# Kernel optimization log

Hardware: AMD Instinct MI355X
Metric: run time of the kernel (lower is better)

The kernel has to match this reference:

```python
import jax, jax.numpy as jnp
import numpy as np

B, N, D, O, L = 16, 2000, 128, 64, 3  # batch, n_nodes, hidden_dim, output_dim, n_layers


def _init(key, shape, fan_in):
    return jax.random.normal(key, shape, jnp.float32) / np.sqrt(fan_in).astype(np.float32)


def setup_inputs() -> dict:
    key = jax.random.key(0)
    ks = jax.random.split(key, 8)
    return {
        "coords": jax.random.normal(ks[0], (B, N, 2), jnp.float32),
        "enc_w0": _init(ks[1], (2, D), 2),
        "enc_b0": jnp.zeros((D,), jnp.float32),
        "enc_w1": _init(ks[2], (D, D), D),
        "enc_b1": jnp.zeros((D,), jnp.float32),
        "gat_W": _init(ks[3], (L, D, D), D),      # per-layer GAT projection (no bias)
        "gat_a1": _init(ks[4], (L, D), 2 * D),    # first half of attention vector a
        "gat_a2": _init(ks[5], (L, D), 2 * D),    # second half of attention vector a
        "proj_w": _init(ks[6], (D, O), D),
        "proj_b": jnp.zeros((O,), jnp.float32),
    }


def _leaky(x):
    return jnp.where(x >= 0, x, 0.2 * x)  # LeakyReLU(0.2)


def reference(coords, enc_w0, enc_b0, enc_w1, enc_b1, gat_W, gat_a1, gat_a2, proj_w, proj_b):
    # node encoder: Linear -> ReLU -> Linear
    h = jax.nn.relu(coords @ enc_w0 + enc_b0) @ enc_w1 + enc_b1  # [B,N,D]
    n_layers = gat_W.shape[0]
    for l in range(n_layers):
        Wh = h @ gat_W[l]                      # [B,N,D]
        # additive GAT attention: e_ij = leakyrelu(a1.Wh_i + a2.Wh_j)
        # (equivalent to a([Wh_i || Wh_j]) without materializing N*N*2D tensor)
        e1 = Wh @ gat_a1[l]                    # [B,N]
        e2 = Wh @ gat_a2[l]                    # [B,N]
        e = _leaky(e1[:, :, None] + e2[:, None, :])  # [B,N,N]
        # adj is all-ones in forward() so the masked_fill is a no-op
        att = jax.nn.softmax(e, axis=-1)       # [B,N,N]; dropout is identity (eval)
        h = jax.nn.relu(att @ Wh)              # [B,N,D]
    return h @ proj_w + proj_b                 # [B,N,O]
```

## Files before the change

kernel.cpp:

```cpp
#include <hip/hip_runtime.h>
#include <hip/hip_bf16.h>

using bf16 = __hip_bfloat16;

#define BATCH 16
#define NNODE 2000
#define DIM   128
#define ODIM  64
#define NLAYER 3
#define BN    (BATCH*NNODE)
#define NP1   (NNODE+1)
#define CHK   125
#define CKS   16

#define OFF_COORDS 0
#define OFF_EW0    64000
#define OFF_EB0    64256
#define OFF_EW1    64384
#define OFF_EB1    80768
#define OFF_GW     80896
#define OFF_GA1    130048
#define OFF_GA2    130432
#define OFF_PW     130816
#define OFF_PB     139008
#define CVT_TOT    139072

struct InPtrs { const void* p[10]; };

__global__ void convert_all_k(InPtrs in, float* __restrict__ dst, float* __restrict__ flag)
{
    __shared__ int scnt[256];
    const unsigned short* raw = (const unsigned short*)in.p[0];
    int t = threadIdx.x, c = 0;
    for (int k = t; k < 2048; k += 256){
        unsigned short u = raw[2*k];
        int e = (u >> 7) & 0xFF;
        if (e >= 100 && e <= 140) ++c;
    }
    scnt[t] = c;
    __syncthreads();
    for (int s = 128; s; s >>= 1){ if (t < s) scnt[t] += scnt[t+s]; __syncthreads(); }
    const bool isbf16 = (scnt[0] >= 1800);
    if (blockIdx.x == 0 && t == 0) flag[0] = isbf16 ? 1.0f : 0.0f;

    const int off[11] = {OFF_COORDS,OFF_EW0,OFF_EB0,OFF_EW1,OFF_EB1,
                         OFF_GW,OFF_GA1,OFF_GA2,OFF_PW,OFF_PB,CVT_TOT};
    int i = blockIdx.x*256 + t;
    if (i >= CVT_TOT) return;
    int seg = 0;
    #pragma unroll
    for (int s = 1; s < 10; ++s) if (i >= off[s]) seg = s;
    int li = i - off[seg];
    if (isbf16) dst[i] = __bfloat162float(((const bf16*)in.p[seg])[li]);
    else        dst[i] = ((const float*)in.p[seg])[li];
}

__global__ __launch_bounds__(256) void encgemm_k(const float* __restrict__ cvt,
                                                 float* __restrict__ out)
{
    __shared__ __align__(16) float sW[128*64];
    __shared__ __align__(16) float sA[32*128];
    const int rt = blockIdx.x, cb = blockIdx.y, tid = threadIdx.x;
    const float* W      = cvt + OFF_EW1;
    const float* bias   = cvt + OFF_EB1;
    const float* coords = cvt + OFF_COORDS;
    const float* w0     = cvt + OFF_EW0;
    const float* b0v    = cvt + OFF_EB0;

    for (int e = tid; e < 128*64; e += 256){
        int k = e >> 6, cc = e & 63;
        sW[e] = W[k*DIM + cb*64 + cc];
    }
    for (int e = tid; e < 32*128; e += 256){
        int r = e >> 7, k = e & 127;
        int node = rt*32 + r;
        float c0 = coords[node*2+0], c1 = coords[node*2+1];
        float v = fmaf(c0, w0[k], fmaf(c1, w0[DIM+k], b0v[k]));
        sA[e] = v > 0.f ? v : 0.f;
    }
    __syncthreads();

    const int cq = tid & 15, rr = tid >> 4;
    float4 acc0 = make_float4(0.f,0.f,0.f,0.f);
    float4 acc1 = make_float4(0.f,0.f,0.f,0.f);
    for (int kq = 0; kq < 32; ++kq){
        float4 w0q = *(float4*)&sW[(kq*4+0)*64 + cq*4];
        float4 w1q = *(float4*)&sW[(kq*4+1)*64 + cq*4];
        float4 w2q = *(float4*)&sW[(kq*4+2)*64 + cq*4];
        float4 w3q = *(float4*)&sW[(kq*4+3)*64 + cq*4];
        float4 a0 = *(float4*)&sA[rr*128 + kq*4];
        float4 a1 = *(float4*)&sA[(rr+16)*128 + kq*4];
        acc0.x = fmaf(a0.x,w0q.x, fmaf(a0.y,w1q.x, fmaf(a0.z,w2q.x, fmaf(a0.w,w3q.x, acc0.x))));
        acc0.y = fmaf(a0.x,w0q.y, fmaf(a0.y,w1q.y, fmaf(a0.z,w2q.y, fmaf(a0.w,w3q.y, acc0.y))));
        acc0.z = fmaf(a0.x,w0q.z, fmaf(a0.y,w1q.z, fmaf(a0.z,w2q.z, fmaf(a0.w,w3q.z, acc0.z))));
        acc0.w = fmaf(a0.x,w0q.w, fmaf(a0.y,w1q.w, fmaf(a0.z,w2q.w, fmaf(a0.w,w3q.w, acc0.w))));
        acc1.x = fmaf(a1.x,w0q.x, fmaf(a1.y,w1q.x, fmaf(a1.z,w2q.x, fmaf(a1.w,w3q.x, acc1.x))));
        acc1.y = fmaf(a1.x,w0q.y, fmaf(a1.y,w1q.y, fmaf(a1.z,w2q.y, fmaf(a1.w,w3q.y, acc1.y))));
        acc1.z = fmaf(a1.x,w0q.z, fmaf(a1.y,w1q.z, fmaf(a1.z,w2q.z, fmaf(a1.w,w3q.z, acc1.z))));
        acc1.w = fmaf(a1.x,w0q.w, fmaf(a1.y,w1q.w, fmaf(a1.z,w2q.w, fmaf(a1.w,w3q.w, acc1.w))));
    }
    const int col0 = cb*64 + cq*4;
    float b0=bias[col0], b1=bias[col0+1], b2=bias[col0+2], b3=bias[col0+3];
    int r0 = rt*32 + rr;
    *(float4*)&out[(size_t)r0*DIM + col0]      = make_float4(acc0.x+b0, acc0.y+b1, acc0.z+b2, acc0.w+b3);
    *(float4*)&out[(size_t)(r0+16)*DIM + col0] = make_float4(acc1.x+b0, acc1.y+b1, acc1.z+b2, acc1.w+b3);
}

__global__ __launch_bounds__(256) void gatgemm_k(const float* __restrict__ A,
    const float* __restrict__ W, const float* __restrict__ a1, const float* __restrict__ a2,
    float* __restrict__ out, float* __restrict__ e1p, float* __restrict__ e2p)
{
    __shared__ __align__(16) float sW[128*64];
    __shared__ __align__(16) float sA[32*128];
    const int rt = blockIdx.x, cb = blockIdx.y, tid = threadIdx.x;

    for (int e = tid; e < 128*64; e += 256){
        int k = e >> 6, cc = e & 63;
        sW[e] = W[k*DIM + cb*64 + cc];
    }
    const float4* Ab = (const float4*)(A + (size_t)rt*32*128);
    float4* sA4 = (float4*)sA;
    for (int q = tid; q < 32*32; q += 256) sA4[q] = Ab[q];
    __syncthreads();

    const int cq = tid & 15, rr = tid >> 4;
    float4 acc0 = make_float4(0.f,0.f,0.f,0.f);
    float4 acc1 = make_float4(0.f,0.f,0.f,0.f);
    for (int kq = 0; kq < 32; ++kq){
        float4 w0q = *(float4*)&sW[(kq*4+0)*64 + cq*4];
        float4 w1q = *(float4*)&sW[(kq*4+1)*64 + cq*4];
        float4 w2q = *(float4*)&sW[(kq*4+2)*64 + cq*4];
        float4 w3q = *(float4*)&sW[(kq*4+3)*64 + cq*4];
        float4 a0 = *(float4*)&sA[rr*128 + kq*4];
        float4 a1q = *(float4*)&sA[(rr+16)*128 + kq*4];
        acc0.x = fmaf(a0.x,w0q.x, fmaf(a0.y,w1q.x, fmaf(a0.z,w2q.x, fmaf(a0.w,w3q.x, acc0.x))));
        acc0.y = fmaf(a0.x,w0q.y, fmaf(a0.y,w1q.y, fmaf(a0.z,w2q.y, fmaf(a0.w,w3q.y, acc0.y))));
        acc0.z = fmaf(a0.x,w0q.z, fmaf(a0.y,w1q.z, fmaf(a0.z,w2q.z, fmaf(a0.w,w3q.z, acc0.z))));
        acc0.w = fmaf(a0.x,w0q.w, fmaf(a0.y,w1q.w, fmaf(a0.z,w2q.w, fmaf(a0.w,w3q.w, acc0.w))));
        acc1.x = fmaf(a1q.x,w0q.x, fmaf(a1q.y,w1q.x, fmaf(a1q.z,w2q.x, fmaf(a1q.w,w3q.x, acc1.x))));
        acc1.y = fmaf(a1q.x,w0q.y, fmaf(a1q.y,w1q.y, fmaf(a1q.z,w2q.y, fmaf(a1q.w,w3q.y, acc1.y))));
        acc1.z = fmaf(a1q.x,w0q.z, fmaf(a1q.y,w1q.z, fmaf(a1q.z,w2q.z, fmaf(a1q.w,w3q.z, acc1.z))));
        acc1.w = fmaf(a1q.x,w0q.w, fmaf(a1q.y,w1q.w, fmaf(a1q.z,w2q.w, fmaf(a1q.w,w3q.w, acc1.w))));
    }
    const int col0 = cb*64 + cq*4;
    int r0 = rt*32 + rr;
    *(float4*)&out[(size_t)r0*DIM + col0]      = acc0;
    *(float4*)&out[(size_t)(r0+16)*DIM + col0] = acc1;

    float a1v0=a1[col0], a1v1=a1[col0+1], a1v2=a1[col0+2], a1v3=a1[col0+3];
    float a2v0=a2[col0], a2v1=a2[col0+1], a2v2=a2[col0+2], a2v3=a2[col0+3];
    float p1r0 = acc0.x*a1v0 + acc0.y*a1v1 + acc0.z*a1v2 + acc0.w*a1v3;
    float p2r0 = acc0.x*a2v0 + acc0.y*a2v1 + acc0.z*a2v2 + acc0.w*a2v3;
    float p1r1 = acc1.x*a1v0 + acc1.y*a1v1 + acc1.z*a1v2 + acc1.w*a1v3;
    float p2r1 = acc1.x*a2v0 + acc1.y*a2v1 + acc1.z*a2v2 + acc1.w*a2v3;
    #pragma unroll
    for (int msk = 1; msk < 16; msk <<= 1){
        p1r0 += __shfl_xor(p1r0, msk); p2r0 += __shfl_xor(p2r0, msk);
        p1r1 += __shfl_xor(p1r1, msk); p2r1 += __shfl_xor(p2r1, msk);
    }
    if (cq == 0){
        e1p[cb*BN + r0]    = p1r0;  e2p[cb*BN + r0]    = p2r0;
        e1p[cb*BN + r0+16] = p1r1;  e2p[cb*BN + r0+16] = p2r1;
    }
}

__global__ __launch_bounds__(256) void gemmout_k(const float* __restrict__ A,
    const float* __restrict__ W, const float* __restrict__ bias,
    void* __restrict__ outp, const float* __restrict__ flag)
{
    __shared__ __align__(16) float sW[128*64];
    __shared__ __align__(16) float sA[32*128];
    const int rt = blockIdx.x, tid = threadIdx.x;
    for (int e = tid; e < 128*64; e += 256){
        int k = e >> 6, cc = e & 63;
        sW[e] = W[k*ODIM + cc];
    }
    const float4* Ab = (const float4*)(A + (size_t)rt*32*128);
    float4* sA4 = (float4*)sA;
    for (int q = tid; q < 32*32; q += 256) sA4[q] = Ab[q];
    __syncthreads();

    const int cq = tid & 15, rr = tid >> 4;
    float4 acc0 = make_float4(0.f,0.f,0.f,0.f);
    float4 acc1 = make_float4(0.f,0.f,0.f,0.f);
    for (int kq = 0; kq < 32; ++kq){
        float4 w0q = *(float4*)&sW[(kq*4+0)*64 + cq*4];
        float4 w1q = *(float4*)&sW[(kq*4+1)*64 + cq*4];
        float4 w2q = *(float4*)&sW[(kq*4+2)*64 + cq*4];
        float4 w3q = *(float4*)&sW[(kq*4+3)*64 + cq*4];
        float4 a0 = *(float4*)&sA[rr*128 + kq*4];
        float4 a1 = *(float4*)&sA[(rr+16)*128 + kq*4];
        acc0.x = fmaf(a0.x,w0q.x, fmaf(a0.y,w1q.x, fmaf(a0.z,w2q.x, fmaf(a0.w,w3q.x, acc0.x))));
        acc0.y = fmaf(a0.x,w0q.y, fmaf(a0.y,w1q.y, fmaf(a0.z,w2q.y, fmaf(a0.w,w3q.y, acc0.y))));
        acc0.z = fmaf(a0.x,w0q.z, fmaf(a0.y,w1q.z, fmaf(a0.z,w2q.z, fmaf(a0.w,w3q.z, acc0.z))));
        acc0.w = fmaf(a0.x,w0q.w, fmaf(a0.y,w1q.w, fmaf(a0.z,w2q.w, fmaf(a0.w,w3q.w, acc0.w))));
        acc1.x = fmaf(a1.x,w0q.x, fmaf(a1.y,w1q.x, fmaf(a1.z,w2q.x, fmaf(a1.w,w3q.x, acc1.x))));
        acc1.y = fmaf(a1.x,w0q.y, fmaf(a1.y,w1q.y, fmaf(a1.z,w2q.y, fmaf(a1.w,w3q.y, acc1.y))));
        acc1.z = fmaf(a1.x,w0q.z, fmaf(a1.y,w1q.z, fmaf(a1.z,w2q.z, fmaf(a1.w,w3q.z, acc1.z))));
        acc1.w = fmaf(a1.x,w0q.w, fmaf(a1.y,w1q.w, fmaf(a1.z,w2q.w, fmaf(a1.w,w3q.w, acc1.w))));
    }
    const int col0 = cq*4;
    float b0=bias[col0], b1=bias[col0+1], b2=bias[col0+2], b3=bias[col0+3];
    float o0[4] = {acc0.x+b0, acc0.y+b1, acc0.z+b2, acc0.w+b3};
    float o1[4] = {acc1.x+b0, acc1.y+b1, acc1.z+b2, acc1.w+b3};
    int r0 = rt*32 + rr;
    size_t p0 = (size_t)r0*ODIM + col0, p1 = (size_t)(r0+16)*ODIM + col0;
    if (flag[0] != 0.0f){
        bf16* ob = (bf16*)outp;
        #pragma unroll
        for (int i = 0; i < 4; ++i){ ob[p0+i] = __float2bfloat16(o0[i]); ob[p1+i] = __float2bfloat16(o1[i]); }
    } else {
        float* of = (float*)outp;
        *(float4*)&of[p0] = make_float4(o0[0],o0[1],o0[2],o0[3]);
        *(float4*)&of[p1] = make_float4(o1[0],o1[1],o1[2],o1[3]);
    }
}

#define WAVE_FENCE() __asm__ volatile("" ::: "memory")
__global__ void sort_k(const float* __restrict__ e2p, float* __restrict__ e2s, int* __restrict__ sidx,
                       float* __restrict__ wp, float* __restrict__ wn, float* __restrict__ e2m)
{
    __shared__ float v[2048];
    __shared__ int  ix[2048];
    const int b = blockIdx.x, t = threadIdx.x;
    for (int i = t; i < 2048; i += 1024){
        v[i]  = (i < NNODE) ? (e2p[b*NNODE + i] + e2p[BN + b*NNODE + i]) : 3.0e38f;
        ix[i] = i;
    }
    __syncthreads();

    #pragma unroll 1
    for (int size = 2; size <= 128; size <<= 1){
        #pragma unroll 1
        for (int stride = size >> 1; stride > 0; stride >>= 1){
            int i = 2*t - (t & (stride-1));
            int j = i + stride;
            bool asc = ((i & size) == 0);
            float vi = v[i], vj = v[j];
            bool sw = asc ? (vi > vj) : (vi < vj);
            if (sw){ v[i]=vj; v[j]=vi; int tm=ix[i]; ix[i]=ix[j]; ix[j]=tm; }
            WAVE_FENCE();
        }
    }
    __syncthreads();

    #pragma unroll 1
    for (int size = 256; size <= 2048; size <<= 1){
        #pragma unroll 1
        for (int stride = size >> 1; stride >= 128; stride >>= 1){
            int i = 2*t - (t & (stride-1));
            int j = i + stride;
            bool asc = ((i & size) == 0);
            float vi = v[i], vj = v[j];
            bool sw = asc ? (vi > vj) : (vi < vj);
            if (sw){ v[i]=vj; v[j]=vi; int tm=ix[i]; ix[i]=ix[j]; ix[j]=tm; }
            __syncthreads();
        }
        #pragma unroll 1
        for (int stride = 64; stride > 0; stride >>= 1){
            int i = 2*t - (t & (stride-1));
            int j = i + stride;
            bool asc = ((i & size) == 0);
            float vi = v[i], vj = v[j];
            bool sw = asc ? (vi > vj) : (vi < vj);
            if (sw){ v[i]=vj; v[j]=vi; int tm=ix[i]; ix[i]=ix[j]; ix[j]=tm; }
            WAVE_FENCE();
        }
        __syncthreads();
    }

    float mx = v[NNODE-1];
    for (int i = t; i < NNODE; i += 1024){
        float val = v[i];
        e2s [b*NNODE+i] = val;
        sidx[b*NNODE+i] = ix[i];
        wp  [b*NNODE+i] = __expf(val - mx);
        wn  [b*NNODE+i] = __expf(0.2f*(val - mx));
    }
    if (t == 0) e2m[b] = mx;
}

__global__ void passA_k(const float* __restrict__ Wh, const int* __restrict__ sidx,
    const float* __restrict__ wp, const float* __restrict__ wn,
    float* __restrict__ chunkP, float* __restrict__ chunkN,
    float* __restrict__ schunkP, float* __restrict__ schunkN)
{
    const int b = blockIdx.x / CHK, c = blockIdx.x % CHK, d = threadIdx.x;
    const int base = b*NNODE;
    float sp=0.f, sn=0.f, ssp=0.f, ssn=0.f;
    #pragma unroll 4
    for (int r = c*CKS; r < c*CKS + CKS; ++r){
        int j = sidx[base + r];
        float whv = Wh[((size_t)base + j)*DIM + d];
        float wpv = wp[base + r], wnv = wn[base + r];
        sp = fmaf(wpv, whv, sp);  sn = fmaf(wnv, whv, sn);
        ssp += wpv;  ssn += wnv;
    }
    const int idx = b*CHK + c;
    chunkP[idx*DIM + d] = sp;
    chunkN[idx*DIM + d] = sn;
    if (d == 0){ schunkP[idx] = ssp; schunkN[idx] = ssn; }
}

__global__ __launch_bounds__(256) void passB_k(
    const float* __restrict__ chunkP, const float* __restrict__ chunkN,
    const float* __restrict__ schunkP, const float* __restrict__ schunkN,
    float* __restrict__ offP, float* __restrict__ offN,
    float* __restrict__ soffP, float* __restrict__ soffN)
{
    const int b = blockIdx.x, tid = threadIdx.x;
    const bool doP = (blockIdx.y == 0);
    const float* chunk  = doP ? chunkP  : chunkN;
    const float* schunk = doP ? schunkP : schunkN;
    float* off  = doP ? offP  : offN;
    float* soff = doP ? soffP : soffN;

    if (tid < 128){
        const int d = tid;
        float acc = 0.f, v[25];
        #pragma unroll
        for (int t = 0; t < 5; ++t){
            const int c0 = doP ? (4-t)*25 : t*25;
            #pragma unroll
            for (int k = 0; k < 25; ++k) v[k] = chunk[(b*CHK + c0 + k)*DIM + d];
            if (doP){
                #pragma unroll
                for (int k = 24; k >= 0; --k){ off[(b*CHK + c0 + k)*DIM + d] = acc; acc += v[k]; }
            } else {
                #pragma unroll
                for (int k = 0; k < 25; ++k){ off[(b*CHK + c0 + k)*DIM + d] = acc; acc += v[k]; }
            }
        }
    } else if (tid == 128){
        float sacc = 0.f, sv[25];
        #pragma unroll
        for (int t = 0; t < 5; ++t){
            const int c0 = doP ? (4-t)*25 : t*25;
            #pragma unroll
            for (int k = 0; k < 25; ++k) sv[k] = schunk[b*CHK + c0 + k];
            if (doP){
                #pragma unroll
                for (int k = 24; k >= 0; --k){ soff[b*CHK + c0 + k] = sacc; sacc += sv[k]; }
            } else {
                #pragma unroll
                for (int k = 0; k < 25; ++k){ soff[b*CHK + c0 + k] = sacc; sacc += sv[k]; }
            }
        }
    }
}

__global__ void passC_k(const float* __restrict__ Wh, const int* __restrict__ sidx,
    const float* __restrict__ wp, const float* __restrict__ wn,
    const float* __restrict__ offP, const float* __restrict__ offN,
    const float* __restrict__ soffP, const float* __restrict__ soffN,
    float* __restrict__ Ppos, float* __restrict__ Pneg,
    float* __restrict__ pposs, float* __restrict__ pnegs)
{
    const int b = blockIdx.x / CHK, c = blockIdx.x % CHK, d = threadIdx.x;
    const int base = b*NNODE;
    const size_t pb = (size_t)b*NP1;
    const int idx = b*CHK + c;
    const int r0 = c*CKS, r1 = r0 + CKS;

    if (c == CHK-1){
        Ppos[(pb + NNODE)*DIM + d] = 0.f;
        if (d == 0) pposs[pb + NNODE] = 0.f;
    }
    float pr = offP[idx*DIM + d], spr = soffP[idx];
    for (int r = r1-1; r >= r0; --r){
        int j = sidx[base + r];
        float whv = Wh[((size_t)base + j)*DIM + d];
        float wpv = wp[base + r];
        pr  = fmaf(wpv, whv, pr);
        spr += wpv;
        Ppos[(pb + r)*DIM + d] = pr;
        if (d == 0) pposs[pb + r] = spr;
    }
    float nr = offN[idx*DIM + d], snr = soffN[idx];
    for (int r = r0; r < r1; ++r){
        int j = sidx[base + r];
        float whv = Wh[((size_t)base + j)*DIM + d];
        float wnv = wn[base + r];
        Pneg[(pb + r)*DIM + d] = nr;
        if (d == 0) pnegs[pb + r] = snr;
        nr  = fmaf(wnv, whv, nr);
        snr += wnv;
    }
    if (c == CHK-1){
        Pneg[(pb + NNODE)*DIM + d] = nr;
        if (d == 0) pnegs[pb + NNODE] = snr;
    }
}

__global__ __launch_bounds__(128) void out16_k(const float* __restrict__ e1p,
    const float* __restrict__ e2s, const float* __restrict__ e2m,
    const float* __restrict__ Ppos, const float* __restrict__ Pneg,
    const float* __restrict__ pposs, const float* __restrict__ pnegs, float* __restrict__ h)
{
    __shared__ int   slo[CKS];
    __shared__ float sps[CKS], sns[CKS];
    const int b = blockIdx.x / CHK, c = blockIdx.x % CHK, d = threadIdx.x;
    const int base = b*NNODE, r0 = c*CKS;
    const size_t pb = (size_t)b*NP1;

    if (d < CKS){
        int row = base + r0 + d;
        float e1v = e1p[row] + e1p[BN + row];
        float s = e1v + e2m[b];
        float m = (s >= 0.f) ? s : 0.2f*s;
        sps[d] = __expf(s - m);
        sns[d] = __expf(0.2f*s - m);
        const float* es = e2s + base;
        float t = -e1v;
        int lo = 0, hi = NNODE;
        while (lo < hi){ int mid = (lo+hi) >> 1; if (es[mid] < t) lo = mid+1; else hi = mid; }
        slo[d] = lo;
    }
    __syncthreads();
    #pragma unroll 4
    for (int k = 0; k < CKS; ++k){
        int row = base + r0 + k;
        size_t kb = pb + slo[k];
        float numer = sps[k]*Ppos[kb*DIM + d] + sns[k]*Pneg[kb*DIM + d];
        float Z     = sps[k]*pposs[kb]        + sns[k]*pnegs[kb];
        float q = numer / Z;
        h[(size_t)row*DIM + d] = (q > 0.f) ? q : ((q == q) ? 0.f : q);
    }
}

extern "C" void kernel_launch(void* const* d_in, const int* in_sizes, int n_in,
                              void* d_out, int out_size, void* d_ws, size_t ws_size,
                              hipStream_t stream)
{
    (void)in_sizes; (void)n_in; (void)out_size; (void)ws_size;

    float* f = (float*)d_ws;
    float* flag    = f;  f += 4;
    float* cvt     = f;  f += CVT_TOT;
    float* h       = f;  f += (size_t)BN*DIM;
    float* Wh      = f;  f += (size_t)BN*DIM;
    float* Ppos    = f;  f += (size_t)BATCH*NP1*DIM;
    float* Pneg    = f;  f += (size_t)BATCH*NP1*DIM;
    float* chunkP  = f;  f += BATCH*CHK*DIM;
    float* chunkN  = f;  f += BATCH*CHK*DIM;
    float* offP    = f;  f += BATCH*CHK*DIM;
    float* offN    = f;  f += BATCH*CHK*DIM;
    float* schunkP = f;  f += BATCH*CHK;
    float* schunkN = f;  f += BATCH*CHK;
    float* soffP   = f;  f += BATCH*CHK;
    float* soffN   = f;  f += BATCH*CHK;
    float* e1p     = f;  f += 2*BN;
    float* e2p     = f;  f += 2*BN;
    float* e2s     = f;  f += BN;
    float* wp      = f;  f += BN;
    float* wn      = f;  f += BN;
    float* pposs   = f;  f += BATCH*NP1;
    float* pnegs   = f;  f += BATCH*NP1;
    float* e2m     = f;  f += 16;
    int*   sidx    = (int*)f;

    InPtrs ip;
    for (int i = 0; i < 10; ++i) ip.p[i] = d_in[i];
    convert_all_k<<<(CVT_TOT+255)/256, 256, 0, stream>>>(ip, cvt, flag);

    encgemm_k<<<dim3(BN/32, 2), 256, 0, stream>>>(cvt, h);

    for (int l = 0; l < NLAYER; ++l){
        gatgemm_k<<<dim3(BN/32, 2), 256, 0, stream>>>(h, cvt + OFF_GW + l*DIM*DIM,
                                                      cvt + OFF_GA1 + l*DIM, cvt + OFF_GA2 + l*DIM,
                                                      Wh, e1p, e2p);
        sort_k<<<BATCH, 1024, 0, stream>>>(e2p, e2s, sidx, wp, wn, e2m);
        passA_k<<<BATCH*CHK, DIM, 0, stream>>>(Wh, sidx, wp, wn, chunkP, chunkN, schunkP, schunkN);
        passB_k<<<dim3(BATCH, 2), 256, 0, stream>>>(chunkP, chunkN, schunkP, schunkN,
                                                    offP, offN, soffP, soffN);
        passC_k<<<BATCH*CHK, DIM, 0, stream>>>(Wh, sidx, wp, wn, offP, offN, soffP, soffN,
                                               Ppos, Pneg, pposs, pnegs);
        out16_k<<<BATCH*CHK, DIM, 0, stream>>>(e1p, e2s, e2m, Ppos, Pneg, pposs, pnegs, h);
    }

    gemmout_k<<<BN/32, 256, 0, stream>>>(h, cvt + OFF_PW, cvt + OFF_PB, d_out, flag);
}
```

Measured before the change: 355.3 us.

## Use split-bf16 MFMA for dense GEMMs and precompute W·a attention vectors

Replaces the scalar fp32 FMA GEMMs for the encoder, the per-layer GAT projection and the output projection with MFMA kernels. Each fp32 operand is split into high and low bf16 parts and three MFMAs per tile pair recover near-fp32 accuracy. A new prep kernel packs the weights once per call and precomputes W@a1 and W@a2. The attention logits e1 and e2 can then come straight from h, which removes the partial-sum buffers and the cross-block shuffle reduction. In exchange it adds a small prep launch, splitting overhead and a small precision change from the three-term bf16 approximation.

```diff
diff --git a/kernel.cpp b/kernel.cpp
--- a/kernel.cpp
+++ b/kernel.cpp
@@ -25,6 +25,24 @@
 #define OFF_PB     139008
 #define CVT_TOT    139072
 
+#define PK_ENC     0
+#define PK_GAT(l)  (32768 + (l)*32768)
+#define PK_PROJ    131072
+#define PK_TOT     147456
+
+typedef __attribute__((ext_vector_type(8))) short bf16x8;
+typedef __attribute__((ext_vector_type(4))) float f32x4;
+
+__device__ __forceinline__ unsigned short f2bf(float f){
+    union { float f; unsigned u; } x; x.f = f;
+    unsigned r = (x.u + 0x7FFFu + ((x.u >> 16) & 1u)) >> 16;
+    return (unsigned short)r;
+}
+__device__ __forceinline__ float bf2f(unsigned short h){
+    union { unsigned u; float f; } x; x.u = ((unsigned)h) << 16;
+    return x.f;
+}
+
 struct InPtrs { const void* p[10]; };
 
 __global__ void convert_all_k(InPtrs in, float* __restrict__ dst, float* __restrict__ flag)
@@ -55,164 +73,252 @@
     else        dst[i] = ((const float*)in.p[seg])[li];
 }
 
-__global__ __launch_bounds__(256) void encgemm_k(const float* __restrict__ cvt,
-                                                 float* __restrict__ out)
-{
-    __shared__ __align__(16) float sW[128*64];
-    __shared__ __align__(16) float sA[32*128];
-    const int rt = blockIdx.x, cb = blockIdx.y, tid = threadIdx.x;
-    const float* W      = cvt + OFF_EW1;
-    const float* bias   = cvt + OFF_EB1;
+__global__ __launch_bounds__(256) void prep_k(const float* __restrict__ cvt,
+                                              unsigned short* __restrict__ pk,
+                                              float* __restrict__ wa)
+{
+    const int mi = blockIdx.x, t = threadIdx.x;
+    const float* W; unsigned short* dst; int N;
+    if (mi == 0)      { W = cvt + OFF_EW1;                    dst = pk + PK_ENC;      N = 128; }
+    else if (mi <= 3) { W = cvt + OFF_GW + (mi-1)*DIM*DIM;    dst = pk + PK_GAT(mi-1);N = 128; }
+    else              { W = cvt + OFF_PW;                     dst = pk + PK_PROJ;     N = 64;  }
+    const int tot = 128*N;
+    unsigned short* dh = dst;
+    unsigned short* dl = dst + tot;
+    for (int e = t; e < tot; e += 256){
+        int col = e >> 7, k = e & 127;
+        float v = W[k*N + col];
+        unsigned short hb = f2bf(v);
+        unsigned short lb = f2bf(v - bf2f(hb));
+        dh[e] = hb;
+        dl[e] = lb;
+    }
+    if (mi >= 1 && mi <= 3){
+        const int l = mi - 1;
+        const float* av = cvt + ((t < 128) ? OFF_GA1 : OFF_GA2) + l*DIM;
+        const int r = t & 127;
+        float s = 0.f;
+        for (int c2 = 0; c2 < 128; ++c2) s = fmaf(W[r*128 + c2], av[c2], s);
+        wa[l*256 + (t >> 7)*128 + r] = s;
+    }
+}
+
+
+__global__ __launch_bounds__(256) void encmfma_k(const float* __restrict__ cvt,
+    const unsigned short* __restrict__ pk, float* __restrict__ h)
+{
+    __shared__ unsigned short sAh[64*128], sAl[64*128];
+    const int t = threadIdx.x, r0 = blockIdx.x*64;
+    const int wv = t >> 6, l = t & 63, lc = l & 15, lk = l >> 4;
+    const unsigned short* ph = pk;
+    const unsigned short* pl = pk + 16384;
+    bf16x8 bh[2][4], bl[2][4];
+    #pragma unroll
+    for (int cg = 0; cg < 2; ++cg){
+        const int col = wv*32 + cg*16 + lc;
+        #pragma unroll
+        for (int kc = 0; kc < 4; ++kc){
+            const int k0 = kc*32 + lk*8;
+            bh[cg][kc] = *(const bf16x8*)&ph[col*128 + k0];
+            bl[cg][kc] = *(const bf16x8*)&pl[col*128 + k0];
+        }
+    }
+    const int row = t >> 2, g = t & 3;
     const float* coords = cvt + OFF_COORDS;
-    const float* w0     = cvt + OFF_EW0;
-    const float* b0v    = cvt + OFF_EB0;
-
-    for (int e = tid; e < 128*64; e += 256){
-        int k = e >> 6, cc = e & 63;
-        sW[e] = W[k*DIM + cb*64 + cc];
-    }
-    for (int e = tid; e < 32*128; e += 256){
-        int r = e >> 7, k = e & 127;
-        int node = rt*32 + r;
-        float c0 = coords[node*2+0], c1 = coords[node*2+1];
-        float v = fmaf(c0, w0[k], fmaf(c1, w0[DIM+k], b0v[k]));
-        sA[e] = v > 0.f ? v : 0.f;
-    }
-    __syncthreads();
-
-    const int cq = tid & 15, rr = tid >> 4;
-    float4 acc0 = make_float4(0.f,0.f,0.f,0.f);
-    float4 acc1 = make_float4(0.f,0.f,0.f,0.f);
-    for (int kq = 0; kq < 32; ++kq){
-        float4 w0q = *(float4*)&sW[(kq*4+0)*64 + cq*4];
-        float4 w1q = *(float4*)&sW[(kq*4+1)*64 + cq*4];
-        float4 w2q = *(float4*)&sW[(kq*4+2)*64 + cq*4];
-        float4 w3q = *(float4*)&sW[(kq*4+3)*64 + cq*4];
-        float4 a0 = *(float4*)&sA[rr*128 + kq*4];
-        float4 a1 = *(float4*)&sA[(rr+16)*128 + kq*4];
-        acc0.x = fmaf(a0.x,w0q.x, fmaf(a0.y,w1q.x, fmaf(a0.z,w2q.x, fmaf(a0.w,w3q.x, acc0.x))));
-        acc0.y = fmaf(a0.x,w0q.y, fmaf(a0.y,w1q.y, fmaf(a0.z,w2q.y, fmaf(a0.w,w3q.y, acc0.y))));
-        acc0.z = fmaf(a0.x,w0q.z, fmaf(a0.y,w1q.z, fmaf(a0.z,w2q.z, fmaf(a0.w,w3q.z, acc0.z))));
-        acc0.w = fmaf(a0.x,w0q.w, fmaf(a0.y,w1q.w, fmaf(a0.z,w2q.w, fmaf(a0.w,w3q.w, acc0.w))));
-        acc1.x = fmaf(a1.x,w0q.x, fmaf(a1.y,w1q.x, fmaf(a1.z,w2q.x, fmaf(a1.w,w3q.x, acc1.x))));
-        acc1.y = fmaf(a1.x,w0q.y, fmaf(a1.y,w1q.y, fmaf(a1.z,w2q.y, fmaf(a1.w,w3q.y, acc1.y))));
-        acc1.z = fmaf(a1.x,w0q.z, fmaf(a1.y,w1q.z, fmaf(a1.z,w2q.z, fmaf(a1.w,w3q.z, acc1.z))));
-        acc1.w = fmaf(a1.x,w0q.w, fmaf(a1.y,w1q.w, fmaf(a1.z,w2q.w, fmaf(a1.w,w3q.w, acc1.w))));
-    }
-    const int col0 = cb*64 + cq*4;
-    float b0=bias[col0], b1=bias[col0+1], b2=bias[col0+2], b3=bias[col0+3];
-    int r0 = rt*32 + rr;
-    *(float4*)&out[(size_t)r0*DIM + col0]      = make_float4(acc0.x+b0, acc0.y+b1, acc0.z+b2, acc0.w+b3);
-    *(float4*)&out[(size_t)(r0+16)*DIM + col0] = make_float4(acc1.x+b0, acc1.y+b1, acc1.z+b2, acc1.w+b3);
-}
-
-__global__ __launch_bounds__(256) void gatgemm_k(const float* __restrict__ A,
-    const float* __restrict__ W, const float* __restrict__ a1, const float* __restrict__ a2,
-    float* __restrict__ out, float* __restrict__ e1p, float* __restrict__ e2p)
-{
-    __shared__ __align__(16) float sW[128*64];
-    __shared__ __align__(16) float sA[32*128];
-    const int rt = blockIdx.x, cb = blockIdx.y, tid = threadIdx.x;
-
-    for (int e = tid; e < 128*64; e += 256){
-        int k = e >> 6, cc = e & 63;
-        sW[e] = W[k*DIM + cb*64 + cc];
-    }
-    const float4* Ab = (const float4*)(A + (size_t)rt*32*128);
-    float4* sA4 = (float4*)sA;
-    for (int q = tid; q < 32*32; q += 256) sA4[q] = Ab[q];
-    __syncthreads();
-
-    const int cq = tid & 15, rr = tid >> 4;
-    float4 acc0 = make_float4(0.f,0.f,0.f,0.f);
-    float4 acc1 = make_float4(0.f,0.f,0.f,0.f);
-    for (int kq = 0; kq < 32; ++kq){
-        float4 w0q = *(float4*)&sW[(kq*4+0)*64 + cq*4];
-        float4 w1q = *(float4*)&sW[(kq*4+1)*64 + cq*4];
-        float4 w2q = *(float4*)&sW[(kq*4+2)*64 + cq*4];
-        float4 w3q = *(float4*)&sW[(kq*4+3)*64 + cq*4];
-        float4 a0 = *(float4*)&sA[rr*128 + kq*4];
-        float4 a1q = *(float4*)&sA[(rr+16)*128 + kq*4];
-        acc0.x = fmaf(a0.x,w0q.x, fmaf(a0.y,w1q.x, fmaf(a0.z,w2q.x, fmaf(a0.w,w3q.x, acc0.x))));
-        acc0.y = fmaf(a0.x,w0q.y, fmaf(a0.y,w1q.y, fmaf(a0.z,w2q.y, fmaf(a0.w,w3q.y, acc0.y))));
-        acc0.z = fmaf(a0.x,w0q.z, fmaf(a0.y,w1q.z, fmaf(a0.z,w2q.z, fmaf(a0.w,w3q.z, acc0.z))));
-        acc0.w = fmaf(a0.x,w0q.w, fmaf(a0.y,w1q.w, fmaf(a0.z,w2q.w, fmaf(a0.w,w3q.w, acc0.w))));
-        acc1.x = fmaf(a1q.x,w0q.x, fmaf(a1q.y,w1q.x, fmaf(a1q.z,w2q.x, fmaf(a1q.w,w3q.x, acc1.x))));
-        acc1.y = fmaf(a1q.x,w0q.y, fmaf(a1q.y,w1q.y, fmaf(a1q.z,w2q.y, fmaf(a1q.w,w3q.y, acc1.y))));
-        acc1.z = fmaf(a1q.x,w0q.z, fmaf(a1q.y,w1q.z, fmaf(a1q.z,w2q.z, fmaf(a1q.w,w3q.z, acc1.z))));
-        acc1.w = fmaf(a1q.x,w0q.w, fmaf(a1q.y,w1q.w, fmaf(a1q.z,w2q.w, fmaf(a1q.w,w3q.w, acc1.w))));
-    }
-    const int col0 = cb*64 + cq*4;
-    int r0 = rt*32 + rr;
-    *(float4*)&out[(size_t)r0*DIM + col0]      = acc0;
-    *(float4*)&out[(size_t)(r0+16)*DIM + col0] = acc1;
-
-    float a1v0=a1[col0], a1v1=a1[col0+1], a1v2=a1[col0+2], a1v3=a1[col0+3];
-    float a2v0=a2[col0], a2v1=a2[col0+1], a2v2=a2[col0+2], a2v3=a2[col0+3];
-    float p1r0 = acc0.x*a1v0 + acc0.y*a1v1 + acc0.z*a1v2 + acc0.w*a1v3;
-    float p2r0 = acc0.x*a2v0 + acc0.y*a2v1 + acc0.z*a2v2 + acc0.w*a2v3;
-    float p1r1 = acc1.x*a1v0 + acc1.y*a1v1 + acc1.z*a1v2 + acc1.w*a1v3;
-    float p2r1 = acc1.x*a2v0 + acc1.y*a2v1 + acc1.z*a2v2 + acc1.w*a2v3;
-    #pragma unroll
-    for (int msk = 1; msk < 16; msk <<= 1){
-        p1r0 += __shfl_xor(p1r0, msk); p2r0 += __shfl_xor(p2r0, msk);
-        p1r1 += __shfl_xor(p1r1, msk); p2r1 += __shfl_xor(p2r1, msk);
-    }
-    if (cq == 0){
-        e1p[cb*BN + r0]    = p1r0;  e2p[cb*BN + r0]    = p2r0;
-        e1p[cb*BN + r0+16] = p1r1;  e2p[cb*BN + r0+16] = p2r1;
-    }
-}
-
-__global__ __launch_bounds__(256) void gemmout_k(const float* __restrict__ A,
-    const float* __restrict__ W, const float* __restrict__ bias,
+    const float* w0  = cvt + OFF_EW0;
+    const float* b0v = cvt + OFF_EB0;
+    const int node = r0 + row;
+    const float c0 = coords[2*node], c1 = coords[2*node+1];
+    char* shb = (char*)sAh; char* slb = (char*)sAl;
+    const int swz = (row & 7) << 4;
+    #pragma unroll
+    for (int i = 0; i < 8; ++i){
+        const int ch = g + i*4, k0 = ch*4;
+        float4 wa0 = *(const float4*)&w0[k0];
+        float4 wb0 = *(const float4*)&w0[DIM + k0];
+        float4 bq  = *(const float4*)&b0v[k0];
+        float4 v;
+        v.x = fmaf(c0, wa0.x, fmaf(c1, wb0.x, bq.x)); v.x = v.x > 0.f ? v.x : 0.f;
+        v.y = fmaf(c0, wa0.y, fmaf(c1, wb0.y, bq.y)); v.y = v.y > 0.f ? v.y : 0.f;
+        v.z = fmaf(c0, wa0.z, fmaf(c1, wb0.z, bq.z)); v.z = v.z > 0.f ? v.z : 0.f;
+        v.w = fmaf(c0, wa0.w, fmaf(c1, wb0.w, bq.w)); v.w = v.w > 0.f ? v.w : 0.f;
+        ushort4 hq, lq;
+        hq.x = f2bf(v.x); lq.x = f2bf(v.x - bf2f(hq.x));
+        hq.y = f2bf(v.y); lq.y = f2bf(v.y - bf2f(hq.y));
+        hq.z = f2bf(v.z); lq.z = f2bf(v.z - bf2f(hq.z));
+        hq.w = f2bf(v.w); lq.w = f2bf(v.w - bf2f(hq.w));
+        const int bo = (ch*8) ^ swz;
+        *(ushort4*)(shb + row*256 + bo) = hq;
+        *(ushort4*)(slb + row*256 + bo) = lq;
+    }
+    __syncthreads();
+    f32x4 acc[4][2] = {};
+    #pragma unroll
+    for (int m = 0; m < 4; ++m){
+        const int ar = m*16 + lc, asw = (ar & 7) << 4;
+        #pragma unroll
+        for (int kc = 0; kc < 4; ++kc){
+            const int bo = (kc*64 + lk*16) ^ asw;
+            bf16x8 ah = *(bf16x8*)(shb + ar*256 + bo);
+            bf16x8 al = *(bf16x8*)(slb + ar*256 + bo);
+            #pragma unroll
+            for (int cg = 0; cg < 2; ++cg){
+                acc[m][cg] = __builtin_amdgcn_mfma_f32_16x16x32_bf16(ah, bh[cg][kc], acc[m][cg], 0, 0, 0);
+                acc[m][cg] = __builtin_amdgcn_mfma_f32_16x16x32_bf16(ah, bl[cg][kc], acc[m][cg], 0, 0, 0);
+                acc[m][cg] = __builtin_amdgcn_mfma_f32_16x16x32_bf16(al, bh[cg][kc], acc[m][cg], 0, 0, 0);
+            }
+        }
+    }
+    const float* eb1 = cvt + OFF_EB1;
+    #pragma unroll
+    for (int m = 0; m < 4; ++m){
+        const int rg = r0 + m*16 + lk*4;
+        #pragma unroll
+        for (int cg = 0; cg < 2; ++cg){
+            const int col = wv*32 + cg*16 + lc;
+            const float bb = eb1[col];
+            #pragma unroll
+            for (int j = 0; j < 4; ++j) h[(size_t)(rg+j)*DIM + col] = acc[m][cg][j] + bb;
+        }
+    }
+}
+
+__global__ __launch_bounds__(256) void gatmfma_k(const float* __restrict__ A,
+    const unsigned short* __restrict__ pk, const float* __restrict__ wa,
+    float* __restrict__ Wh, float* __restrict__ e1p, float* __restrict__ e2p)
+{
+    __shared__ unsigned short sAh[64*128], sAl[64*128];
+    const int t = threadIdx.x, r0 = blockIdx.x*64;
+    const int wv = t >> 6, l = t & 63, lc = l & 15, lk = l >> 4;
+    const unsigned short* ph = pk;
+    const unsigned short* pl = pk + 16384;
+    bf16x8 bh[2][4], bl[2][4];
+    #pragma unroll
+    for (int cg = 0; cg < 2; ++cg){
+        const int col = wv*32 + cg*16 + lc;
+        #pragma unroll
+        for (int kc = 0; kc < 4; ++kc){
+            const int k0 = kc*32 + lk*8;
+            bh[cg][kc] = *(const bf16x8*)&ph[col*128 + k0];
+            bl[cg][kc] = *(const bf16x8*)&pl[col*128 + k0];
+        }
+    }
+    const int row = t >> 2, g = t & 3;
+    const float* Ar = A + (size_t)(r0 + row)*DIM;
+    char* shb = (char*)sAh; char* slb = (char*)sAl;
+    const int swz = (row & 7) << 4;
+    float e1 = 0.f, e2 = 0.f;
+    #pragma unroll
+    for (int i = 0; i < 8; ++i){
+        const int ch = g + i*4;
+        float4 a  = *(const float4*)&Ar[ch*4];
+        float4 u1 = *(const float4*)&wa[ch*4];
+        float4 u2 = *(const float4*)&wa[128 + ch*4];
+        e1 = fmaf(a.x,u1.x, fmaf(a.y,u1.y, fmaf(a.z,u1.z, fmaf(a.w,u1.w, e1))));
+        e2 = fmaf(a.x,u2.x, fmaf(a.y,u2.y, fmaf(a.z,u2.z, fmaf(a.w,u2.w, e2))));
+        ushort4 hq, lq;
+        hq.x = f2bf(a.x); lq.x = f2bf(a.x - bf2f(hq.x));
+        hq.y = f2bf(a.y); lq.y = f2bf(a.y - bf2f(hq.y));
+        hq.z = f2bf(a.z); lq.z = f2bf(a.z - bf2f(hq.z));
+        hq.w = f2bf(a.w); lq.w = f2bf(a.w - bf2f(hq.w));
+        const int bo = (ch*8) ^ swz;
+        *(ushort4*)(shb + row*256 + bo) = hq;
+        *(ushort4*)(slb + row*256 + bo) = lq;
+    }
+    e1 += __shfl_xor(e1, 1); e1 += __shfl_xor(e1, 2);
+    e2 += __shfl_xor(e2, 1); e2 += __shfl_xor(e2, 2);
+    if (g == 0){ e1p[r0 + row] = e1; e2p[r0 + row] = e2; }
+    __syncthreads();
+    f32x4 acc[4][2] = {};
+    #pragma unroll
+    for (int m = 0; m < 4; ++m){
+        const int ar = m*16 + lc, asw = (ar & 7) << 4;
+        #pragma unroll
+        for (int kc = 0; kc < 4; ++kc){
+            const int bo = (kc*64 + lk*16) ^ asw;
+            bf16x8 ah = *(bf16x8*)(shb + ar*256 + bo);
+            bf16x8 al = *(bf16x8*)(slb + ar*256 + bo);
+            #pragma unroll
+            for (int cg = 0; cg < 2; ++cg){
+                acc[m][cg] = __builtin_amdgcn_mfma_f32_16x16x32_bf16(ah, bh[cg][kc], acc[m][cg], 0, 0, 0);
+                acc[m][cg] = __builtin_amdgcn_mfma_f32_16x16x32_bf16(ah, bl[cg][kc], acc[m][cg], 0, 0, 0);
+                acc[m][cg] = __builtin_amdgcn_mfma_f32_16x16x32_bf16(al, bh[cg][kc], acc[m][cg], 0, 0, 0);
+            }
+        }
+    }
+    #pragma unroll
+    for (int m = 0; m < 4; ++m){
+        const int rg = r0 + m*16 + lk*4;
+        #pragma unroll
+        for (int cg = 0; cg < 2; ++cg){
+            const int col = wv*32 + cg*16 + lc;
+            #pragma unroll
+            for (int j = 0; j < 4; ++j) Wh[(size_t)(rg+j)*DIM + col] = acc[m][cg][j];
+        }
+    }
+}
+
+__global__ __launch_bounds__(256) void projmfma_k(const float* __restrict__ A,
+    const unsigned short* __restrict__ pk, const float* __restrict__ bias,
     void* __restrict__ outp, const float* __restrict__ flag)
 {
-    __shared__ __align__(16) float sW[128*64];
-    __shared__ __align__(16) float sA[32*128];
-    const int rt = blockIdx.x, tid = threadIdx.x;
-    for (int e = tid; e < 128*64; e += 256){
-        int k = e >> 6, cc = e & 63;
-        sW[e] = W[k*ODIM + cc];
-    }
-    const float4* Ab = (const float4*)(A + (size_t)rt*32*128);
-    float4* sA4 = (float4*)sA;
-    for (int q = tid; q < 32*32; q += 256) sA4[q] = Ab[q];
-    __syncthreads();
-
-    const int cq = tid & 15, rr = tid >> 4;
-    float4 acc0 = make_float4(0.f,0.f,0.f,0.f);
-    float4 acc1 = make_float4(0.f,0.f,0.f,0.f);
-    for (int kq = 0; kq < 32; ++kq){
-        float4 w0q = *(float4*)&sW[(kq*4+0)*64 + cq*4];
-        float4 w1q = *(float4*)&sW[(kq*4+1)*64 + cq*4];
-        float4 w2q = *(float4*)&sW[(kq*4+2)*64 + cq*4];
-        float4 w3q = *(float4*)&sW[(kq*4+3)*64 + cq*4];
-        float4 a0 = *(float4*)&sA[rr*128 + kq*4];
-        float4 a1 = *(float4*)&sA[(rr+16)*128 + kq*4];
-        acc0.x = fmaf(a0.x,w0q.x, fmaf(a0.y,w1q.x, fmaf(a0.z,w2q.x, fmaf(a0.w,w3q.x, acc0.x))));
-        acc0.y = fmaf(a0.x,w0q.y, fmaf(a0.y,w1q.y, fmaf(a0.z,w2q.y, fmaf(a0.w,w3q.y, acc0.y))));
-        acc0.z = fmaf(a0.x,w0q.z, fmaf(a0.y,w1q.z, fmaf(a0.z,w2q.z, fmaf(a0.w,w3q.z, acc0.z))));
-        acc0.w = fmaf(a0.x,w0q.w, fmaf(a0.y,w1q.w, fmaf(a0.z,w2q.w, fmaf(a0.w,w3q.w, acc0.w))));
-        acc1.x = fmaf(a1.x,w0q.x, fmaf(a1.y,w1q.x, fmaf(a1.z,w2q.x, fmaf(a1.w,w3q.x, acc1.x))));
-        acc1.y = fmaf(a1.x,w0q.y, fmaf(a1.y,w1q.y, fmaf(a1.z,w2q.y, fmaf(a1.w,w3q.y, acc1.y))));
-        acc1.z = fmaf(a1.x,w0q.z, fmaf(a1.y,w1q.z, fmaf(a1.z,w2q.z, fmaf(a1.w,w3q.z, acc1.z))));
-        acc1.w = fmaf(a1.x,w0q.w, fmaf(a1.y,w1q.w, fmaf(a1.z,w2q.w, fmaf(a1.w,w3q.w, acc1.w))));
-    }
-    const int col0 = cq*4;
-    float b0=bias[col0], b1=bias[col0+1], b2=bias[col0+2], b3=bias[col0+3];
-    float o0[4] = {acc0.x+b0, acc0.y+b1, acc0.z+b2, acc0.w+b3};
-    float o1[4] = {acc1.x+b0, acc1.y+b1, acc1.z+b2, acc1.w+b3};
-    int r0 = rt*32 + rr;
-    size_t p0 = (size_t)r0*ODIM + col0, p1 = (size_t)(r0+16)*ODIM + col0;
-    if (flag[0] != 0.0f){
-        bf16* ob = (bf16*)outp;
-        #pragma unroll
-        for (int i = 0; i < 4; ++i){ ob[p0+i] = __float2bfloat16(o0[i]); ob[p1+i] = __float2bfloat16(o1[i]); }
-    } else {
-        float* of = (float*)outp;
-        *(float4*)&of[p0] = make_float4(o0[0],o0[1],o0[2],o0[3]);
-        *(float4*)&of[p1] = make_float4(o1[0],o1[1],o1[2],o1[3]);
+    __shared__ unsigned short sAh[64*128], sAl[64*128];
+    const int t = threadIdx.x, r0 = blockIdx.x*64;
+    const int wv = t >> 6, l = t & 63, lc = l & 15, lk = l >> 4;
+    const unsigned short* ph = pk;
+    const unsigned short* pl = pk + 8192;
+    bf16x8 bh[4], bl[4];
+    const int col = wv*16 + lc;
+    #pragma unroll
+    for (int kc = 0; kc < 4; ++kc){
+        const int k0 = kc*32 + lk*8;
+        bh[kc] = *(const bf16x8*)&ph[col*128 + k0];
+        bl[kc] = *(const bf16x8*)&pl[col*128 + k0];
+    }
+    const int row = t >> 2, g = t & 3;
+    const float* Ar = A + (size_t)(r0 + row)*DIM;
+    char* shb = (char*)sAh; char* slb = (char*)sAl;
+    const int swz = (row & 7) << 4;
+    #pragma unroll
+    for (int i = 0; i < 8; ++i){
+        const int ch = g + i*4;
+        float4 a = *(const float4*)&Ar[ch*4];
+        ushort4 hq, lq;
+        hq.x = f2bf(a.x); lq.x = f2bf(a.x - bf2f(hq.x));
+        hq.y = f2bf(a.y); lq.y = f2bf(a.y - bf2f(hq.y));
+        hq.z = f2bf(a.z); lq.z = f2bf(a.z - bf2f(hq.z));
+        hq.w = f2bf(a.w); lq.w = f2bf(a.w - bf2f(hq.w));
+        const int bo = (ch*8) ^ swz;
+        *(ushort4*)(shb + row*256 + bo) = hq;
+        *(ushort4*)(slb + row*256 + bo) = lq;
+    }
+    __syncthreads();
+    f32x4 acc[4] = {};
+    #pragma unroll
+    for (int m = 0; m < 4; ++m){
+        const int ar = m*16 + lc, asw = (ar & 7) << 4;
+        #pragma unroll
+        for (int kc = 0; kc < 4; ++kc){
+            const int bo = (kc*64 + lk*16) ^ asw;
+            bf16x8 ah = *(bf16x8*)(shb + ar*256 + bo);
+            bf16x8 al = *(bf16x8*)(slb + ar*256 + bo);
+            acc[m] = __builtin_amdgcn_mfma_f32_16x16x32_bf16(ah, bh[kc], acc[m], 0, 0, 0);
+            acc[m] = __builtin_amdgcn_mfma_f32_16x16x32_bf16(ah, bl[kc], acc[m], 0, 0, 0);
+            acc[m] = __builtin_amdgcn_mfma_f32_16x16x32_bf16(al, bh[kc], acc[m], 0, 0, 0);
+        }
+    }
+    const float bb = bias[col];
+    const bool isbf = (flag[0] != 0.0f);
+    #pragma unroll
+    for (int m = 0; m < 4; ++m){
+        const int rg = r0 + m*16 + lk*4;
+        #pragma unroll
+        for (int j = 0; j < 4; ++j){
+            float v = acc[m][j] + bb;
+            size_t p = (size_t)(rg+j)*ODIM + col;
+            if (isbf) ((bf16*)outp)[p] = __float2bfloat16(v);
+            else      ((float*)outp)[p] = v;
+        }
     }
 }
 
@@ -224,7 +330,7 @@
     __shared__ int  ix[2048];
     const int b = blockIdx.x, t = threadIdx.x;
     for (int i = t; i < 2048; i += 1024){
-        v[i]  = (i < NNODE) ? (e2p[b*NNODE + i] + e2p[BN + b*NNODE + i]) : 3.0e38f;
+        v[i]  = (i < NNODE) ? e2p[b*NNODE + i] : 3.0e38f;
         ix[i] = i;
     }
     __syncthreads();
@@ -405,15 +511,15 @@
 
     if (d < CKS){
         int row = base + r0 + d;
-        float e1v = e1p[row] + e1p[BN + row];
+        float e1v = e1p[row];
         float s = e1v + e2m[b];
         float m = (s >= 0.f) ? s : 0.2f*s;
         sps[d] = __expf(s - m);
         sns[d] = __expf(0.2f*s - m);
         const float* es = e2s + base;
-        float t = -e1v;
+        float tt = -e1v;
         int lo = 0, hi = NNODE;
-        while (lo < hi){ int mid = (lo+hi) >> 1; if (es[mid] < t) lo = mid+1; else hi = mid; }
+        while (lo < hi){ int mid = (lo+hi) >> 1; if (es[mid] < tt) lo = mid+1; else hi = mid; }
         slo[d] = lo;
     }
     __syncthreads();
@@ -449,8 +555,8 @@
     float* schunkN = f;  f += BATCH*CHK;
     float* soffP   = f;  f += BATCH*CHK;
     float* soffN   = f;  f += BATCH*CHK;
-    float* e1p     = f;  f += 2*BN;
-    float* e2p     = f;  f += 2*BN;
+    float* e1p     = f;  f += BN;
+    float* e2p     = f;  f += BN;
     float* e2s     = f;  f += BN;
     float* wp      = f;  f += BN;
     float* wn      = f;  f += BN;
@@ -458,17 +564,19 @@
     float* pnegs   = f;  f += BATCH*NP1;
     float* e2m     = f;  f += 16;
     int*   sidx    = (int*)f;
+    unsigned short* pk = (unsigned short*)(sidx + BN);
+    float* wa      = (float*)(pk + PK_TOT);
 
     InPtrs ip;
     for (int i = 0; i < 10; ++i) ip.p[i] = d_in[i];
     convert_all_k<<<(CVT_TOT+255)/256, 256, 0, stream>>>(ip, cvt, flag);
 
-    encgemm_k<<<dim3(BN/32, 2), 256, 0, stream>>>(cvt, h);
+    prep_k<<<5, 256, 0, stream>>>(cvt, pk, wa);
+
+    encmfma_k<<<BN/64, 256, 0, stream>>>(cvt, pk + PK_ENC, h);
 
     for (int l = 0; l < NLAYER; ++l){
-        gatgemm_k<<<dim3(BN/32, 2), 256, 0, stream>>>(h, cvt + OFF_GW + l*DIM*DIM,
-                                                      cvt + OFF_GA1 + l*DIM, cvt + OFF_GA2 + l*DIM,
-                                                      Wh, e1p, e2p);
+        gatmfma_k<<<BN/64, 256, 0, stream>>>(h, pk + PK_GAT(l), wa + l*256, Wh, e1p, e2p);
         sort_k<<<BATCH, 1024, 0, stream>>>(e2p, e2s, sidx, wp, wn, e2m);
         passA_k<<<BATCH*CHK, DIM, 0, stream>>>(Wh, sidx, wp, wn, chunkP, chunkN, schunkP, schunkN);
         passB_k<<<dim3(BATCH, 2), 256, 0, stream>>>(chunkP, chunkN, schunkP, schunkN,
@@ -478,5 +586,5 @@
         out16_k<<<BATCH*CHK, DIM, 0, stream>>>(e1p, e2s, e2m, Ppos, Pneg, pposs, pnegs, h);
     }
 
-    gemmout_k<<<BN/32, 256, 0, stream>>>(h, cvt + OFF_PW, cvt + OFF_PB, d_out, flag);
-}
+    projmfma_k<<<BN/64, 256, 0, stream>>>(h, pk + PK_PROJ, cvt + OFF_PB, d_out, flag);
+}
```

After: 310.4 us. 12.6% less time.
